# Performance work log

Measured on AMD Instinct MI355X. Metric: run time of the kernel, lower is better.

Reference implementation:

```python
import jax, jax.numpy as jnp
import numpy as np
from jax import lax

REGION_SIZE = 5      # local window side (init kwarg)
BANDWIDTH = 0.1      # KDE kernel bandwidth (init kwarg)
NUM_BINS = 256       # intensity histogram bins
EPS = 1e-10


def setup_inputs() -> dict:
    key = jax.random.key(0)
    # image-like inputs in [0, 255] to match the 256 intensity bins
    x = jax.random.uniform(key, (8, 3, 96, 96), dtype=jnp.float32) * 255.0
    return {"x": x}


def reference(x):
    # x: [B, C, H, W]
    bins = jnp.arange(NUM_BINS, dtype=x.dtype)            # [256]
    # derivative-of-sigmoid KDE kernel evaluated at each (pixel, bin) pair
    d = (x[..., None] - bins) / BANDWIDTH                 # [B,C,H,W,256]
    sig = jax.nn.sigmoid(d)
    k = sig * (1.0 - sig)                                 # [B,C,H,W,256]
    # accumulate kernel mass over the region_size x region_size window
    # (stride 1, centered -> SAME padding), per bin
    p = lax.reduce_window(
        k, jnp.float32(0.0), lax.add,
        window_dimensions=(1, 1, REGION_SIZE, REGION_SIZE, 1),
        window_strides=(1, 1, 1, 1, 1),
        padding='SAME')                                   # [B,C,H,W,256]
    # normalize to a probability distribution over bins
    p = p / (jnp.sum(p, axis=-1, keepdims=True) + EPS)
    # Shannon entropy per pixel
    return -jnp.sum(p * jnp.log(p + EPS), axis=-1)        # [B,C,H,W]
```

## Files before the change

### kernel.cpp

```cpp
#include <hip/hip_runtime.h>
#include <hip/hip_fp16.h>
#include <stdint.h>


#define W 96
#define H 96
#define TPB 256
#define SPLIT 18

template<int NB, int I0>
__device__ __forceinline__ void role_compute(const float* __restrict__ base,
                                             int xcol, int y,
                                             float& Sout, float& Tout)
{
    int b0a[NB]; uint32_t pk[NB];
    float S = 0.f;
    #pragma unroll
    for (int i = 0; i < NB; ++i) {
        const int dy = i / 5 - 2, dx = i % 5 - 2;
        const int yy = y + dy,    xx = xcol + dx;
        const bool ok = (yy >= 0) & (yy < H) & (xx >= 0) & (xx < W);
        const float v  = base[min(max(yy, 0), H - 1) * W + min(max(xx, 0), W - 1)];
        const int   b0 = (int)v;
        const float f  = v - (float)b0;
        const float E  = __expf(-10.f * f);
        const float E2 = __expf(10.f * f - 10.f);
        const float r0 = __builtin_amdgcn_rcpf(1.f + E);
        const float r1 = __builtin_amdgcn_rcpf(1.f + E2);
        const float k0 = ok ? E  * r0 * r0 : 0.f;
        const float k1 = ok ? E2 * r1 * r1 : 0.f;
        const __half2 hk = __floats2half2_rn(k0, k1);
        if (i >= I0) {
            const float2 kc = __half22float2(hk);
            S += kc.x + kc.y;
        }
        b0a[i] = b0;
        pk[i]  = __builtin_bit_cast(uint32_t, hk);
    }

    float T0 = 0.f, T1 = 0.f;
    #pragma unroll
    for (int i = I0; i < NB; ++i) {
        const int b0i = b0a[i];
        uint32_t Ppk = 0u;
        #pragma unroll
        for (int j = 0; j < i; ++j) {
            const int d = b0i - b0a[j];
            int s = 16 * d + 32;
            s = s < 0 ? 0 : (s > 63 ? 63 : s);
            const uint32_t t = (uint32_t)((((uint64_t)pk[j]) << 32) >> s);
            const __half2 sum = __hadd2(__builtin_bit_cast(__half2, Ppk),
                                        __builtin_bit_cast(__half2, t));
            Ppk = __builtin_bit_cast(uint32_t, sum);
        }
        const float2 P  = __half22float2(__builtin_bit_cast(__half2, Ppk));
        const float2 kc = __half22float2(__builtin_bit_cast(__half2, pk[i]));
        const float z0 = P.x + kc.x, z1 = P.y + kc.y;
        const float t4 = z0 * __logf(z0 + 1e-10f) - P.x * __logf(P.x + 1e-10f)
                       + z1 * __logf(z1 + 1e-10f) - P.y * __logf(P.y + 1e-10f);
        if (i & 1) T1 += t4; else T0 += t4;
    }
    Sout = S;
    Tout = T0 + T1;
}

__global__ __launch_bounds__(TPB) void entropy_kde_kernel(
    const float* __restrict__ x, float* __restrict__ out, int total)
{
    __shared__ float sS[128], sT[128];
    const int tid  = threadIdx.x;
    const int wv   = tid >> 6;
    const int g    = wv >> 1;
    const int r    = wv & 1;
    const int l    = tid & 63;
    const int slot = g * 64 + l;
    const int px   = blockIdx.x * 128 + slot;

    const int xcol = px % W;
    const int y    = (px / W) % H;
    const int img  = px / (W * H);
    const float* __restrict__ base = x + img * (H * W);

    float S, T;
    if (r == 0) role_compute<SPLIT, 0>(base, xcol, y, S, T);
    else        role_compute<25, SPLIT>(base, xcol, y, S, T);

    if (r == 1) { sS[slot] = S; sT[slot] = T; }
    __syncthreads();
    if (r == 0) {
        S += sS[slot];
        T += sT[slot];
        const float Sp = S + 1e-10f;
        if (px < total) out[px] = __logf(Sp) - T / Sp;
    }
}

extern "C" void kernel_launch(void* const* d_in, const int* in_sizes, int n_in,
                              void* d_out, int out_size, void* d_ws, size_t ws_size,
                              hipStream_t stream)
{
    const float* x = (const float*)d_in[0];
    float* out = (float*)d_out;
    const int total  = in_sizes[0];
    const int blocks = total / 128;
    entropy_kde_kernel<<<blocks, TPB, 0, stream>>>(x, out, total);
}
```

Measured before the change: 80.73 us.

## Precompute per-pixel kernel mass in a separate pass and gather it

Adds a pre-pass kernel that computes each pixel's two half-precision kernel values and bin index once, storing them in workspace as uint2. The main kernel then gathers these precomputed values for its 25 window neighbours instead of recomputing exponentials and reciprocals for each one. This removes the roughly 25x redundant transcendental work. In exchange it adds a second kernel launch and an 8-byte-per-pixel workspace round trip through memory.

```diff
diff --git a/kernel.cpp b/kernel.cpp
--- a/kernel.cpp
+++ b/kernel.cpp
@@ -8,8 +8,26 @@
 #define TPB 256
 #define SPLIT 18
 
+__global__ __launch_bounds__(TPB) void mass_kernel(
+    const float* __restrict__ x, uint2* __restrict__ wm, int total)
+{
+    const int pid = blockIdx.x * TPB + threadIdx.x;
+    if (pid >= total) return;
+    const float v  = x[pid];
+    const int   b0 = (int)v;
+    const float f  = v - (float)b0;
+    const float E  = __expf(-10.f * f);
+    const float E2 = __expf(10.f * f - 10.f);
+    const float r0 = __builtin_amdgcn_rcpf(1.f + E);
+    const float r1 = __builtin_amdgcn_rcpf(1.f + E2);
+    const float k0 = E  * r0 * r0;
+    const float k1 = E2 * r1 * r1;
+    const __half2 hk = __floats2half2_rn(k0, k1);
+    wm[pid] = make_uint2(__builtin_bit_cast(uint32_t, hk), (uint32_t)b0);
+}
+
 template<int NB, int I0>
-__device__ __forceinline__ void role_compute(const float* __restrict__ base,
+__device__ __forceinline__ void role_compute(const uint2* __restrict__ wb,
                                              int xcol, int y,
                                              float& Sout, float& Tout)
 {
@@ -20,22 +38,13 @@
         const int dy = i / 5 - 2, dx = i % 5 - 2;
         const int yy = y + dy,    xx = xcol + dx;
         const bool ok = (yy >= 0) & (yy < H) & (xx >= 0) & (xx < W);
-        const float v  = base[min(max(yy, 0), H - 1) * W + min(max(xx, 0), W - 1)];
-        const int   b0 = (int)v;
-        const float f  = v - (float)b0;
-        const float E  = __expf(-10.f * f);
-        const float E2 = __expf(10.f * f - 10.f);
-        const float r0 = __builtin_amdgcn_rcpf(1.f + E);
-        const float r1 = __builtin_amdgcn_rcpf(1.f + E2);
-        const float k0 = ok ? E  * r0 * r0 : 0.f;
-        const float k1 = ok ? E2 * r1 * r1 : 0.f;
-        const __half2 hk = __floats2half2_rn(k0, k1);
+        const uint2 m = wb[min(max(yy, 0), H - 1) * W + min(max(xx, 0), W - 1)];
+        pk[i]  = ok ? m.x : 0u;
+        b0a[i] = (int)m.y;
         if (i >= I0) {
-            const float2 kc = __half22float2(hk);
+            const float2 kc = __half22float2(__builtin_bit_cast(__half2, pk[i]));
             S += kc.x + kc.y;
         }
-        b0a[i] = b0;
-        pk[i]  = __builtin_bit_cast(uint32_t, hk);
     }
 
     float T0 = 0.f, T1 = 0.f;
@@ -65,7 +74,7 @@
 }
 
 __global__ __launch_bounds__(TPB) void entropy_kde_kernel(
-    const float* __restrict__ x, float* __restrict__ out, int total)
+    const uint2* __restrict__ wm, float* __restrict__ out, int total)
 {
     __shared__ float sS[128], sT[128];
     const int tid  = threadIdx.x;
@@ -79,11 +88,11 @@
     const int xcol = px % W;
     const int y    = (px / W) % H;
     const int img  = px / (W * H);
-    const float* __restrict__ base = x + img * (H * W);
+    const uint2* __restrict__ wb = wm + img * (H * W);
 
     float S, T;
-    if (r == 0) role_compute<SPLIT, 0>(base, xcol, y, S, T);
-    else        role_compute<25, SPLIT>(base, xcol, y, S, T);
+    if (r == 0) role_compute<SPLIT, 0>(wb, xcol, y, S, T);
+    else        role_compute<25, SPLIT>(wb, xcol, y, S, T);
 
     if (r == 1) { sS[slot] = S; sT[slot] = T; }
     __syncthreads();
@@ -101,7 +110,8 @@
 {
     const float* x = (const float*)d_in[0];
     float* out = (float*)d_out;
-    const int total  = in_sizes[0];
-    const int blocks = total / 128;
-    entropy_kde_kernel<<<blocks, TPB, 0, stream>>>(x, out, total);
+    uint2* wm  = (uint2*)d_ws;
+    const int total = in_sizes[0];
+    mass_kernel<<<(total + TPB - 1) / TPB, TPB, 0, stream>>>(x, wm, total);
+    entropy_kde_kernel<<<total / 128, TPB, 0, stream>>>(wm, out, total);
 }
```

Result: faster. 77.61 us (-3.9%).
